# Optimization experiments

Measured on AMD Instinct MI355X. Metric: run time of the kernel, lower is better.

Reference implementation:

```python
import jax, jax.numpy as jnp
import numpy as np

DIM = 4096
N_HEADS = 32
N_KV_HEADS = 8
HEAD_DIM = 128
ROPE_THETA = 10000.0
REPEATS = N_HEADS // N_KV_HEADS
SCALE = HEAD_DIM ** -0.5


def rope(x, seq_len, offset):
    # x: [b, h, seq_len, head_dim]; faithful to source: cos/sin from cat((freqs,freqs)),
    # rotate built by interleaved pair swap then flatten.
    d = x.shape[-1]
    inv_freq = 1.0 / (ROPE_THETA ** (jnp.arange(0, d, 2, dtype=jnp.float32) / d))  # [d/2]
    t = jnp.arange(offset, offset + seq_len, dtype=jnp.float32)                    # [L]
    freqs = t[:, None] * inv_freq[None, :]                                         # [L, d/2]
    emb = jnp.concatenate([freqs, freqs], axis=-1)                                 # [L, d]
    cos_emb = jnp.cos(emb)
    sin_emb = jnp.sin(emb)
    x_even = x[..., 0::2]
    x_odd = x[..., 1::2]
    rotate_x = jnp.stack([-x_odd, x_even], axis=-1).reshape(x.shape)
    return x * cos_emb + rotate_x * sin_emb


def setup_inputs() -> dict:
    key = jax.random.key(0)
    k1, k2, k3, k4, k5 = jax.random.split(key, 5)
    b, l = 1, 2048
    s = 0.02
    x = jax.random.normal(k1, (b, l, DIM), dtype=jnp.float32)
    wq = jax.random.normal(k2, (DIM, N_HEADS * HEAD_DIM), dtype=jnp.float32) * s
    wk = jax.random.normal(k3, (DIM, N_KV_HEADS * HEAD_DIM), dtype=jnp.float32) * s
    wv = jax.random.normal(k4, (DIM, N_KV_HEADS * HEAD_DIM), dtype=jnp.float32) * s
    wo = jax.random.normal(k5, (N_HEADS * HEAD_DIM, DIM), dtype=jnp.float32) * s
    return {"x": x, "wq": wq, "wk": wk, "wv": wv, "wo": wo, "seq_len": l}


def reference(x, wq, wk, wv, wo, seq_len):
    b, l, _ = x.shape
    q = (x @ wq).reshape(b, l, N_HEADS, HEAD_DIM).transpose(0, 2, 1, 3)       # [b,H,l,d]
    k = (x @ wk).reshape(b, l, N_KV_HEADS, HEAD_DIM).transpose(0, 2, 1, 3)    # [b,Hk,l,d]
    v = (x @ wv).reshape(b, l, N_KV_HEADS, HEAD_DIM).transpose(0, 2, 1, 3)
    # repeat KV heads to match query heads (GQA)
    k = jnp.repeat(k, REPEATS, axis=1)   # [b,H,l,d]
    v = jnp.repeat(v, REPEATS, axis=1)
    offset = 0  # cache is None
    q = rope(q, seq_len, offset)
    k = rope(k, seq_len, offset)
    scores = jnp.einsum('bhid,bhjd->bhij', q * SCALE, k)
    scores = jax.nn.softmax(scores.astype(jnp.float32), axis=-1).astype(scores.dtype)
    out = jnp.einsum('bhij,bhjd->bhid', scores, v)
    out = out.transpose(0, 2, 1, 3).reshape(b, l, N_HEADS * HEAD_DIM)
    return out @ wo, (k, v)
```

## Files before the change

### kernel.cpp

```cpp
#include <hip/hip_runtime.h>
#include <cstdint>
#include <cstddef>

#define DIM 4096
#define SEQ 2048
#define NH 32
#define NKV 8
#define HD 128
#define QKVN 6144

typedef __bf16 bf16_t;
typedef __bf16 bf16x8 __attribute__((ext_vector_type(8)));
typedef __bf16 bf16x4 __attribute__((ext_vector_type(4)));
typedef __bf16 bf16x2 __attribute__((ext_vector_type(2)));
typedef float f32x4 __attribute__((ext_vector_type(4)));
typedef int int4v __attribute__((ext_vector_type(4)));

__device__ __forceinline__ f32x4 mfma16(bf16x8 a, bf16x8 b, f32x4 c) {
  return __builtin_amdgcn_mfma_f32_16x16x32_bf16(a, b, c, 0, 0, 0);
}

__device__ __forceinline__ void async16(const bf16_t* g, bf16_t* l) {
  __builtin_amdgcn_global_load_lds((__attribute__((address_space(1))) void*)g,
                                   (__attribute__((address_space(3))) void*)l,
                                   16, 0, 0);
}

__device__ __forceinline__ int pack2(float a, float b) {
  bf16x2 h = { (bf16_t)a, (bf16_t)b };
  return __builtin_bit_cast(int, h);
}

#define LGKM0() do { asm volatile("s_waitcnt lgkmcnt(0)" ::: "memory"); \
                     __builtin_amdgcn_sched_barrier(0); } while (0)

template <int N> __device__ __forceinline__ void vmw() {
  if constexpr (N == 2) asm volatile("s_waitcnt vmcnt(2)" ::: "memory");
  else if constexpr (N == 3) asm volatile("s_waitcnt vmcnt(3)" ::: "memory");
  else if constexpr (N == 4) asm volatile("s_waitcnt vmcnt(4)" ::: "memory");
  __builtin_amdgcn_sched_barrier(0);
}

__global__ void cast_x(const float* __restrict__ x, bf16_t* __restrict__ xb) {
  int i = blockIdx.x * 256 + threadIdx.x;
  const float4 v = ((const float4*)x)[i];
  bf16x4 o = { (bf16_t)v.x, (bf16_t)v.y, (bf16_t)v.z, (bf16_t)v.w };
  *(bf16x4*)(xb + (size_t)i * 4) = o;
}

__global__ void tcast(const float* __restrict__ src, bf16_t* __restrict__ dst,
                      int Ncols, int Kdim) {
  __shared__ float tile[32][33];
  int n0 = blockIdx.x * 32, k0 = blockIdx.y * 32;
  int tx = threadIdx.x, ty = threadIdx.y;
#pragma unroll
  for (int r = 0; r < 4; r++)
    tile[ty + 8 * r][tx] = src[(size_t)(k0 + ty + 8 * r) * Ncols + n0 + tx];
  __syncthreads();
#pragma unroll
  for (int r = 0; r < 4; r++)
    dst[(size_t)(n0 + ty + 8 * r) * Kdim + k0 + tx] = (bf16_t)tile[tx][ty + 8 * r];
}

template <int NF>
__global__ __launch_bounds__(512) void gemm256(const bf16_t* __restrict__ A,
                                               const bf16_t* __restrict__ Bt,
                                               float* __restrict__ C,
                                               int M, int N, int K) {
  __shared__ bf16_t As[2][16384];
  __shared__ bf16_t Bs[2][NF * 4096];
  const int t = threadIdx.x;
  const int lane = t & 63;
  const int l15 = lane & 15, quad = lane >> 4;
  const int w = t >> 6, wm = w >> 2, wn = w & 3;
  const int cgx = l15 & 7;

  const int gx = gridDim.x;
  const int nwg = gx * gridDim.y;
  const int id = blockIdx.y * gx + blockIdx.x;
  const int swz = (id & 7) * (nwg >> 3) + (id >> 3);
  const int bm = (swz / gx) * 256, bn = (swz % gx) * (NF * 64);

  const int srow = t >> 3;
  const int scol = ((t & 7) ^ (srow & 7)) << 3;
  const bf16_t* gA = A + (size_t)(bm + srow) * K + scol;
  const bf16_t* gB = Bt + (size_t)(bn + srow) * K + scol;
  const int ldst = t * 8;

  f32x4 acc[8][NF] = {};

  auto stP0 = [&](int b2, int kk) {
    async16(gA + kk, &As[b2][ldst]);
    async16(gA + (size_t)64 * K + kk, &As[b2][4096 + ldst]);
    if constexpr (NF == 2) {
      async16(gB + kk, &Bs[b2][ldst]);
      async16(gB + (size_t)64 * K + kk, &Bs[b2][4096 + ldst]);
    }
  };
  auto stP1 = [&](int b2, int kk) {
    if constexpr (NF == 3) {
      async16(gB + kk, &Bs[b2][ldst]);
      async16(gB + (size_t)64 * K + kk, &Bs[b2][4096 + ldst]);
    } else {
      async16(gA + (size_t)128 * K + kk, &As[b2][8192 + ldst]);
      async16(gA + (size_t)192 * K + kk, &As[b2][12288 + ldst]);
    }
  };
  auto stP2 = [&](int b2, int kk) {
    async16(gA + (size_t)128 * K + kk, &As[b2][8192 + ldst]);
    async16(gA + (size_t)192 * K + kk, &As[b2][12288 + ldst]);
    async16(gB + (size_t)128 * K + kk, &Bs[b2][8192 + ldst]);
  };

  stP0(0, 0);
  stP1(0, 0);
  if constexpr (NF == 3) stP2(0, 0);
  if constexpr (NF == 3) vmw<3>(); else vmw<2>();
  __builtin_amdgcn_s_barrier();

  const int nkt = K >> 6;
  for (int kt = 0; kt < nkt; ++kt) {
    const int b2 = kt & 1, bo = b2 ^ 1;
    const int kn = (kt + 1 == nkt) ? 0 : (kt + 1) << 6;

    bf16x8 afl[4][2], afh[4][2], bf01[2][2], bf2[2];

#pragma unroll
    for (int mi = 0; mi < 4; mi++)
#pragma unroll
      for (int s = 0; s < 2; s++)
        afl[mi][s] = *(const bf16x8*)&As[b2][(wm * 64 + mi * 16 + l15) * 64 +
                                            ((((s << 2) | quad) ^ cgx) << 3)];
#pragma unroll
    for (int ni = 0; ni < 2; ni++)
#pragma unroll
      for (int s = 0; s < 2; s++)
        bf01[ni][s] = *(const bf16x8*)&Bs[b2][(ni * 64 + wn * 16 + l15) * 64 +
                                              ((((s << 2) | quad) ^ cgx) << 3)];
    stP0(bo, kn);
    __builtin_amdgcn_s_barrier();
    LGKM0();
    __builtin_amdgcn_s_setprio(1);
#pragma unroll
    for (int mi = 0; mi < 4; mi++)
#pragma unroll
      for (int ni = 0; ni < 2; ni++)
#pragma unroll
        for (int s = 0; s < 2; s++)
          acc[mi][ni] = mfma16(afl[mi][s], bf01[ni][s], acc[mi][ni]);
    __builtin_amdgcn_s_setprio(0);
    if constexpr (NF == 3) vmw<3>(); else vmw<4>();
    __builtin_amdgcn_s_barrier();

#pragma unroll
    for (int mi = 0; mi < 4; mi++)
#pragma unroll
      for (int s = 0; s < 2; s++)
        afh[mi][s] = *(const bf16x8*)&As[b2][(128 + wm * 64 + mi * 16 + l15) * 64 +
                                             ((((s << 2) | quad) ^ cgx) << 3)];
    stP1(bo, kn);
    __builtin_amdgcn_s_barrier();
    LGKM0();
    __builtin_amdgcn_s_setprio(1);
#pragma unroll
    for (int mi = 0; mi < 4; mi++)
#pragma unroll
      for (int ni = 0; ni < 2; ni++)
#pragma unroll
        for (int s = 0; s < 2; s++)
          acc[mi + 4][ni] = mfma16(afh[mi][s], bf01[ni][s], acc[mi + 4][ni]);
    __builtin_amdgcn_s_setprio(0);
    if constexpr (NF == 3) vmw<4>(); else vmw<2>();
    __builtin_amdgcn_s_barrier();

    if constexpr (NF == 3) {
#pragma unroll
      for (int s = 0; s < 2; s++)
        bf2[s] = *(const bf16x8*)&Bs[b2][(128 + wn * 16 + l15) * 64 +
                                         ((((s << 2) | quad) ^ cgx) << 3)];
      stP2(bo, kn);
      __builtin_amdgcn_s_barrier();
      LGKM0();
      __builtin_amdgcn_s_setprio(1);
#pragma unroll
      for (int mi = 0; mi < 4; mi++)
#pragma unroll
        for (int s = 0; s < 2; s++) {
          acc[mi][2] = mfma16(afl[mi][s], bf2[s], acc[mi][2]);
          acc[mi + 4][2] = mfma16(afh[mi][s], bf2[s], acc[mi + 4][2]);
        }
      __builtin_amdgcn_s_setprio(0);
      vmw<3>();
      __builtin_amdgcn_s_barrier();
    }
  }

#pragma unroll
  for (int mi = 0; mi < 8; mi++)
#pragma unroll
    for (int ni = 0; ni < NF; ni++) {
      size_t row = (size_t)bm + (mi >> 2) * 128 + wm * 64 + (mi & 3) * 16 + quad * 4;
      size_t col = (size_t)bn + ni * 64 + wn * 16 + l15;
#pragma unroll
      for (int r = 0; r < 4; r++)
        C[(row + r) * N + col] = acc[mi][ni][r];
    }
  asm volatile("s_waitcnt vmcnt(0)" ::: "memory");
}

__global__ void rope_scatter(const float* __restrict__ qkv, bf16_t* __restrict__ Qb,
                             bf16_t* __restrict__ Kb, bf16_t* __restrict__ Vt,
                             float* __restrict__ kOut, float* __restrict__ vOut) {
  int idx = blockIdx.x * 256 + threadIdx.x;
  int t = idx / 3072;
  int p = idx - t * 3072;
  const float NEG_L2T_64 = -0.20762050593046f;
  const float SS = 0.08838834764831845f * 1.4426950408889634f;
  if (p < 2048) {
    int hh = p >> 6, pr = p & 63;
    int d0 = pr << 1;
    const float* src = qkv + (size_t)t * QKVN + hh * HD + d0;
    float a = src[0], b = src[1];
    int j0 = d0 & 63, j1 = (d0 + 1) & 63;
    float th0 = (float)t * exp2f((float)j0 * NEG_L2T_64);
    float th1 = (float)t * exp2f((float)j1 * NEG_L2T_64);
    float o0 = (a * cosf(th0) - b * sinf(th0)) * SS;
    float o1 = (b * cosf(th1) + a * sinf(th1)) * SS;
    bf16_t* dst = Qb + ((size_t)hh * SEQ + t) * HD + d0;
    dst[0] = (bf16_t)o0;
    dst[1] = (bf16_t)o1;
  } else if (p < 2560) {
    int q2 = p - 2048;
    int kh = q2 >> 6, pr = q2 & 63;
    int d0 = pr << 1;
    const float* src = qkv + (size_t)t * QKVN + 4096 + kh * HD + d0;
    float a = src[0], b = src[1];
    int j0 = d0 & 63, j1 = (d0 + 1) & 63;
    float th0 = (float)t * exp2f((float)j0 * NEG_L2T_64);
    float th1 = (float)t * exp2f((float)j1 * NEG_L2T_64);
    float o0 = a * cosf(th0) - b * sinf(th0);
    float o1 = b * cosf(th1) + a * sinf(th1);
    bf16_t* dst = Kb + ((size_t)kh * SEQ + t) * HD + d0;
    dst[0] = (bf16_t)o0;
    dst[1] = (bf16_t)o1;
#pragma unroll
    for (int rep = 0; rep < 4; rep++) {
      float* kp = kOut + ((size_t)(kh * 4 + rep) * SEQ + t) * HD + d0;
      kp[0] = o0;
      kp[1] = o1;
    }
  } else {
    int q2 = p - 2560;
    int kh = q2 >> 6, pr = q2 & 63;
    int d0 = pr << 1;
    const float* src = qkv + (size_t)t * QKVN + 5120 + kh * HD + d0;
    float a = src[0], b = src[1];
#pragma unroll
    for (int rep = 0; rep < 4; rep++) {
      float* vp = vOut + ((size_t)(kh * 4 + rep) * SEQ + t) * HD + d0;
      vp[0] = a;
      vp[1] = b;
    }
    int tp = (t & ~31) + ((t & 12) << 1) + (t & 3) + ((t & 16) >> 2);
    Vt[((size_t)kh * HD + d0) * SEQ + tp] = (bf16_t)a;
    Vt[((size_t)kh * HD + d0 + 1) * SEQ + tp] = (bf16_t)b;
  }
}

__global__ __launch_bounds__(512, 2) void attn_kernel(const bf16_t* __restrict__ Qb,
                                                      const bf16_t* __restrict__ Kb,
                                                      const bf16_t* __restrict__ Vt,
                                                      bf16_t* __restrict__ AO) {
  __shared__ bf16_t Ks[2][8192];
  __shared__ bf16_t Vs[2][8192];
  const int h = blockIdx.y, kh = h >> 2;
  const int qbase = blockIdx.x * 256;
  const int w = threadIdx.x >> 6, lane = threadIdx.x & 63;
  const int l15 = lane & 15, quad = lane >> 4;
  const bf16_t* KbH = Kb + (size_t)kh * SEQ * HD;
  const bf16_t* VtH = Vt + (size_t)kh * HD * SEQ;

  bf16x8 qf[2][4];
#pragma unroll
  for (int nq = 0; nq < 2; nq++) {
    const bf16_t* qp = Qb + ((size_t)h * SEQ + qbase + w * 32 + nq * 16 + l15) * HD + quad * 8;
#pragma unroll
    for (int kc = 0; kc < 4; kc++) qf[nq][kc] = *(const bf16x8*)(qp + kc * 32);
  }

  f32x4 acc[8][2] = {};
  float rsum[2] = {0.f, 0.f};

  auto stage = [&](int buf, int kt0) {
    if (w < 4) {
      int kc = w;
#pragma unroll
      for (int kg = 0; kg < 4; kg++) {
        const bf16_t* g = KbH + (size_t)(kt0 + kg * 16 + (lane >> 2)) * HD + kc * 32 + (lane & 3) * 8;
        async16(g, &Ks[buf][kc * 2048 + kg * 512]);
      }
    } else {
      int vi = w - 4, kt = vi >> 1, dg0 = (vi & 1) * 4;
#pragma unroll
      for (int j = 0; j < 4; j++) {
        int dg = dg0 + j;
        const bf16_t* g = VtH + (size_t)(dg * 16 + (lane >> 2)) * SEQ + kt0 + kt * 32 + (lane & 3) * 8;
        async16(g, &Vs[buf][kt * 4096 + dg * 512]);
      }
    }
  };

  stage(0, 0);
  int buf = 0;

  for (int kt0 = 0; kt0 < SEQ; kt0 += 64, buf ^= 1) {
    __syncthreads();
    if (kt0 + 64 < SEQ) stage(buf ^ 1, kt0 + 64);

    f32x4 sacc[4][2] = {};
#pragma unroll
    for (int mi = 0; mi < 4; mi++)
#pragma unroll
      for (int kc = 0; kc < 4; kc++) {
        bf16x8 kf = *(const bf16x8*)(&Ks[buf][(kc * 64 + mi * 16 + l15) * 32 + quad * 8]);
#pragma unroll
        for (int nq = 0; nq < 2; nq++)
          sacc[mi][nq] = mfma16(kf, qf[nq][kc], sacc[mi][nq]);
      }

    int pk[4][2][2];
#pragma unroll
    for (int mi = 0; mi < 4; mi++)
#pragma unroll
      for (int nq = 0; nq < 2; nq++) {
        float p0 = exp2f(sacc[mi][nq][0]);
        float p1 = exp2f(sacc[mi][nq][1]);
        float p2 = exp2f(sacc[mi][nq][2]);
        float p3 = exp2f(sacc[mi][nq][3]);
        rsum[nq] += (p0 + p1) + (p2 + p3);
        pk[mi][nq][0] = pack2(p0, p1);
        pk[mi][nq][1] = pack2(p2, p3);
      }

#pragma unroll
    for (int kt = 0; kt < 2; kt++) {
#pragma unroll
      for (int nq = 0; nq < 2; nq++) {
        int4v dw;
        dw[0] = pk[2 * kt][nq][0];
        dw[1] = pk[2 * kt][nq][1];
        dw[2] = pk[2 * kt + 1][nq][0];
        dw[3] = pk[2 * kt + 1][nq][1];
        bf16x8 pf = __builtin_bit_cast(bf16x8, dw);
#pragma unroll
        for (int dt = 0; dt < 8; dt++) {
          bf16x8 vf = *(const bf16x8*)(&Vs[buf][(kt * 128 + dt * 16 + l15) * 32 + quad * 8]);
          acc[dt][nq] = mfma16(vf, pf, acc[dt][nq]);
        }
      }
    }
  }

#pragma unroll
  for (int nq = 0; nq < 2; nq++) {
    float rs = rsum[nq];
    rs += __shfl_xor(rs, 16);
    rs += __shfl_xor(rs, 32);
    float inv = 1.0f / rs;
    int q = qbase + w * 32 + nq * 16 + l15;
#pragma unroll
    for (int dt = 0; dt < 8; dt++) {
      bf16x4 o = { (bf16_t)(acc[dt][nq][0] * inv), (bf16_t)(acc[dt][nq][1] * inv),
                   (bf16_t)(acc[dt][nq][2] * inv), (bf16_t)(acc[dt][nq][3] * inv) };
      *(bf16x4*)(AO + (size_t)q * DIM + h * HD + dt * 16 + quad * 4) = o;
    }
  }
}

extern "C" void kernel_launch(void* const* d_in, const int* in_sizes, int n_in,
                              void* d_out, int out_size, void* d_ws, size_t ws_size,
                              hipStream_t stream) {
  const float* x = (const float*)d_in[0];
  const float* wq = (const float*)d_in[1];
  const float* wk = (const float*)d_in[2];
  const float* wv = (const float*)d_in[3];
  const float* wo = (const float*)d_in[4];
  float* out = (float*)d_out;
  float* kOut = out + (size_t)SEQ * DIM;
  float* vOut = kOut + (size_t)NH * SEQ * HD;

  char* ws = (char*)d_ws;
  bf16_t* Xb = (bf16_t*)ws;
  bf16_t* WT = (bf16_t*)(ws + 16777216);
  float* QKV = (float*)(ws + 67108864);
  bf16_t* WoT = (bf16_t*)(ws + 67108864);
  bf16_t* Qb = (bf16_t*)(ws + 117440512);
  bf16_t* Kb = (bf16_t*)(ws + 134217728);
  bf16_t* Vt = (bf16_t*)(ws + 138412032);
  bf16_t* AO = Xb;

  dim3 tb(32, 8);
  cast_x<<<8192, 256, 0, stream>>>(x, Xb);
  tcast<<<dim3(128, 128), tb, 0, stream>>>(wq, WT, 4096, 4096);
  tcast<<<dim3(32, 128), tb, 0, stream>>>(wk, WT + (size_t)4096 * 4096, 1024, 4096);
  tcast<<<dim3(32, 128), tb, 0, stream>>>(wv, WT + (size_t)5120 * 4096, 1024, 4096);
  gemm256<3><<<dim3(32, 8), 512, 0, stream>>>(Xb, WT, QKV, 2048, 6144, 4096);
  rope_scatter<<<24576, 256, 0, stream>>>(QKV, Qb, Kb, Vt, kOut, vOut);
  tcast<<<dim3(128, 128), tb, 0, stream>>>(wo, WoT, 4096, 4096);
  attn_kernel<<<dim3(8, 32), 512, 0, stream>>>(Qb, Kb, Vt, AO);
  gemm256<2><<<dim3(32, 8), 512, 0, stream>>>(AO, WoT, out, 2048, 4096, 4096);
}
```

Baseline: 522.5 us.

## Replace phased GEMM load pipeline with single-stage prefetch and one barrier per tile

The QKV/output GEMM main loop drops the three-phase interleaving of async global-to-LDS loads, partial vmcnt waits and extra barriers. It now issues the whole next k-tile prefetch at the top of each iteration, runs all MFMAs on the current buffer, then does one full vmcnt(0) wait and one barrier. The goal is fewer barriers and less scheduling overhead per tile. The cost is coarser overlap: each iteration ends with a full drain of outstanding loads, and LDS fragment reads are no longer staggered against loads.

```diff
diff --git a/kernel.cpp b/kernel.cpp
--- a/kernel.cpp
+++ b/kernel.cpp
@@ -31,15 +31,8 @@
   return __builtin_bit_cast(int, h);
 }
 
-#define LGKM0() do { asm volatile("s_waitcnt lgkmcnt(0)" ::: "memory"); \
-                     __builtin_amdgcn_sched_barrier(0); } while (0)
-
-template <int N> __device__ __forceinline__ void vmw() {
-  if constexpr (N == 2) asm volatile("s_waitcnt vmcnt(2)" ::: "memory");
-  else if constexpr (N == 3) asm volatile("s_waitcnt vmcnt(3)" ::: "memory");
-  else if constexpr (N == 4) asm volatile("s_waitcnt vmcnt(4)" ::: "memory");
-  __builtin_amdgcn_sched_barrier(0);
-}
+#define VM0() do { asm volatile("s_waitcnt vmcnt(0)" ::: "memory"); \
+                   __builtin_amdgcn_sched_barrier(0); } while (0)
 
 __global__ void cast_x(const float* __restrict__ x, bf16_t* __restrict__ xb) {
   int i = blockIdx.x * 256 + threadIdx.x;
@@ -89,33 +82,19 @@
 
   f32x4 acc[8][NF] = {};
 
-  auto stP0 = [&](int b2, int kk) {
+  auto stage = [&](int b2, int kk) {
     async16(gA + kk, &As[b2][ldst]);
     async16(gA + (size_t)64 * K + kk, &As[b2][4096 + ldst]);
-    if constexpr (NF == 2) {
-      async16(gB + kk, &Bs[b2][ldst]);
-      async16(gB + (size_t)64 * K + kk, &Bs[b2][4096 + ldst]);
-    }
-  };
-  auto stP1 = [&](int b2, int kk) {
-    if constexpr (NF == 3) {
-      async16(gB + kk, &Bs[b2][ldst]);
-      async16(gB + (size_t)64 * K + kk, &Bs[b2][4096 + ldst]);
-    } else {
-      async16(gA + (size_t)128 * K + kk, &As[b2][8192 + ldst]);
-      async16(gA + (size_t)192 * K + kk, &As[b2][12288 + ldst]);
-    }
-  };
-  auto stP2 = [&](int b2, int kk) {
     async16(gA + (size_t)128 * K + kk, &As[b2][8192 + ldst]);
     async16(gA + (size_t)192 * K + kk, &As[b2][12288 + ldst]);
-    async16(gB + (size_t)128 * K + kk, &Bs[b2][8192 + ldst]);
+    async16(gB + kk, &Bs[b2][ldst]);
+    async16(gB + (size_t)64 * K + kk, &Bs[b2][4096 + ldst]);
+    if constexpr (NF == 3)
+      async16(gB + (size_t)128 * K + kk, &Bs[b2][8192 + ldst]);
   };
 
-  stP0(0, 0);
-  stP1(0, 0);
-  if constexpr (NF == 3) stP2(0, 0);
-  if constexpr (NF == 3) vmw<3>(); else vmw<2>();
+  stage(0, 0);
+  VM0();
   __builtin_amdgcn_s_barrier();
 
   const int nkt = K >> 6;
@@ -123,8 +102,9 @@
     const int b2 = kt & 1, bo = b2 ^ 1;
     const int kn = (kt + 1 == nkt) ? 0 : (kt + 1) << 6;
 
+    stage(bo, kn);
+
     bf16x8 afl[4][2], afh[4][2], bf01[2][2], bf2[2];
-
 #pragma unroll
     for (int mi = 0; mi < 4; mi++)
 #pragma unroll
@@ -137,9 +117,7 @@
       for (int s = 0; s < 2; s++)
         bf01[ni][s] = *(const bf16x8*)&Bs[b2][(ni * 64 + wn * 16 + l15) * 64 +
                                               ((((s << 2) | quad) ^ cgx) << 3)];
-    stP0(bo, kn);
-    __builtin_amdgcn_s_barrier();
-    LGKM0();
+
     __builtin_amdgcn_s_setprio(1);
 #pragma unroll
     for (int mi = 0; mi < 4; mi++)
@@ -148,20 +126,12 @@
 #pragma unroll
         for (int s = 0; s < 2; s++)
           acc[mi][ni] = mfma16(afl[mi][s], bf01[ni][s], acc[mi][ni]);
-    __builtin_amdgcn_s_setprio(0);
-    if constexpr (NF == 3) vmw<3>(); else vmw<4>();
-    __builtin_amdgcn_s_barrier();
-
 #pragma unroll
     for (int mi = 0; mi < 4; mi++)
 #pragma unroll
       for (int s = 0; s < 2; s++)
         afh[mi][s] = *(const bf16x8*)&As[b2][(128 + wm * 64 + mi * 16 + l15) * 64 +
                                              ((((s << 2) | quad) ^ cgx) << 3)];
-    stP1(bo, kn);
-    __builtin_amdgcn_s_barrier();
-    LGKM0();
-    __builtin_amdgcn_s_setprio(1);
 #pragma unroll
     for (int mi = 0; mi < 4; mi++)
 #pragma unroll
@@ -169,19 +139,11 @@
 #pragma unroll
         for (int s = 0; s < 2; s++)
           acc[mi + 4][ni] = mfma16(afh[mi][s], bf01[ni][s], acc[mi + 4][ni]);
-    __builtin_amdgcn_s_setprio(0);
-    if constexpr (NF == 3) vmw<4>(); else vmw<2>();
-    __builtin_amdgcn_s_barrier();
-
     if constexpr (NF == 3) {
 #pragma unroll
       for (int s = 0; s < 2; s++)
         bf2[s] = *(const bf16x8*)&Bs[b2][(128 + wn * 16 + l15) * 64 +
                                          ((((s << 2) | quad) ^ cgx) << 3)];
-      stP2(bo, kn);
-      __builtin_amdgcn_s_barrier();
-      LGKM0();
-      __builtin_amdgcn_s_setprio(1);
 #pragma unroll
       for (int mi = 0; mi < 4; mi++)
 #pragma unroll
@@ -189,10 +151,11 @@
           acc[mi][2] = mfma16(afl[mi][s], bf2[s], acc[mi][2]);
           acc[mi + 4][2] = mfma16(afh[mi][s], bf2[s], acc[mi + 4][2]);
         }
-      __builtin_amdgcn_s_setprio(0);
-      vmw<3>();
-      __builtin_amdgcn_s_barrier();
-    }
+    }
+    __builtin_amdgcn_s_setprio(0);
+
+    VM0();
+    __builtin_amdgcn_s_barrier();
   }
 
 #pragma unroll
@@ -205,7 +168,6 @@
       for (int r = 0; r < 4; r++)
         C[(row + r) * N + col] = acc[mi][ni][r];
     }
-  asm volatile("s_waitcnt vmcnt(0)" ::: "memory");
 }
 
 __global__ void rope_scatter(const float* __restrict__ qkv, bf16_t* __restrict__ Qb,
```

After: 553.7 us. +6.0%, slower.
